# Performance work log

Measured on AMD Instinct MI355X. Metric: run time of the kernel, lower is better.

## Reference

```python
import jax, jax.numpy as jnp
import numpy as np

N = 100_000
E = 1_600_000
F_IN, D1, D2, D_EMB = 64, 32, 64, 64
NUM_GRAPHS = 16
BN_EPS = 1e-5


def _glorot(key, shape):
    fan_in, fan_out = shape[0], shape[1]
    lim = (6.0 / (fan_in + fan_out)) ** 0.5
    return jax.random.uniform(key, shape, jnp.float32, -lim, lim)


def setup_inputs() -> dict:
    key = jax.random.key(0)
    ks = jax.random.split(key, 12)
    x = jax.random.normal(ks[0], (N, F_IN), jnp.float32)
    edge_index = jax.random.randint(ks[1], (2, E), 0, N, jnp.int64)
    batch = jnp.sort(jax.random.randint(ks[2], (N,), 0, NUM_GRAPHS, jnp.int64))
    return {
        "x": x,
        "edge_index": edge_index,
        "batch": batch,
        "num_graphs": NUM_GRAPHS,
        "num_nodes": N,
        "W1a": _glorot(ks[3], (F_IN, D1)), "b1a": jnp.zeros((D1,), jnp.float32),
        "W1b": _glorot(ks[4], (D1, D2)), "b1b": jnp.zeros((D2,), jnp.float32),
        "g1": jnp.ones((D2,), jnp.float32), "be1": jnp.zeros((D2,), jnp.float32),
        "W2a": _glorot(ks[5], (D2, D2)), "b2a": jnp.zeros((D2,), jnp.float32),
        "W2b": _glorot(ks[6], (D2, D_EMB)), "b2b": jnp.zeros((D_EMB,), jnp.float32),
        "g2": jnp.ones((D_EMB,), jnp.float32), "be2": jnp.zeros((D_EMB,), jnp.float32),
    }


def _batchnorm_train(h, gamma, beta):
    mean = jnp.mean(h, axis=0)
    var = jnp.mean(jnp.square(h - mean), axis=0)  # biased var, as torch BN uses for normalization
    return (h - mean) * jax.lax.rsqrt(var + BN_EPS) * gamma + beta


def _gin_aggregate(x, src, dst, valid, n_nodes):
    # sum_{j in N(i)} x_j over valid edges only (masked scatter-add)
    msg = x[src] * valid[:, None]  # [E, D]
    return jax.ops.segment_sum(msg, dst, num_segments=n_nodes)


def reference(x, edge_index, batch, num_graphs, num_nodes,
              W1a, b1a, W1b, b1b, g1, be1,
              W2a, b2a, W2b, b2b, g2, be2):
    n_edges = edge_index.shape[1]
    per = n_edges // num_graphs
    # edge_mask: per-edge threshold g * num_nodes / num_graphs applied to both rows
    thresh = jnp.repeat(jnp.arange(num_graphs), per).astype(jnp.float32) * (num_nodes / num_graphs)
    valid = jnp.all(edge_index.astype(jnp.float32) - thresh[None, :] >= 0.0, axis=0)
    valid = valid.astype(x.dtype)
    src, dst = edge_index[0], edge_index[1]

    # GINConv 1 (eps=0): nn1(x + aggr)
    h = x + _gin_aggregate(x, src, dst, valid, num_nodes)
    h = jax.nn.relu(h @ W1a + b1a) @ W1b + b1b
    h = jax.nn.relu(h)
    h = _batchnorm_train(h, g1, be1)

    # GINConv 2
    h = h + _gin_aggregate(h, src, dst, valid, num_nodes)
    h = jax.nn.relu(h @ W2a + b2a) @ W2b + b2b
    h = jax.nn.relu(h)
    h = _batchnorm_train(h, g2, be2)

    # global_mean_pool
    sums = jax.ops.segment_sum(h, batch, num_segments=num_graphs)
    counts = jax.ops.segment_sum(jnp.ones((h.shape[0],), h.dtype), batch, num_segments=num_graphs)
    return sums / jnp.maximum(counts, 1.0)[:, None]
```

## Files before the change

### kernel.cpp

```cpp
#include <hip/hip_runtime.h>
#include <hip/hip_fp16.h>

#define NG 16
#define D 64
#define SLOT 32
#define NPB 128
#define INH 72

union HF4 { float4 f4; __half2 h2[4]; };
union HF2 { float2 f2; __half2 h2[2]; };

typedef _Float16 half4_t __attribute__((ext_vector_type(4)));
typedef float float4_t __attribute__((ext_vector_type(4)));

__device__ __forceinline__ float2 f2fma(float2 a, float2 b, float2 c) {
  return make_float2(fmaf(a.x, b.x, c.x), fmaf(a.y, b.y, c.y));
}
__device__ __forceinline__ float2 f2add(float2 a, float2 b) {
  return make_float2(a.x + b.x, a.y + b.y);
}

__device__ __forceinline__ void load16(const float4* __restrict__ feat4, int N,
                                       int q8, int4 a, int4 b, int4 c, int4 d,
                                       HF4* u) {
  int ix[16] = {a.x, a.y, a.z, a.w, b.x, b.y, b.z, b.w,
                c.x, c.y, c.z, c.w, d.x, d.y, d.z, d.w};
#pragma unroll
  for (int i = 0; i < 16; i++)
    u[i].f4 = feat4[(size_t)min(ix[i], N) * 8 + q8];
}
__device__ __forceinline__ void acc16(const HF4* u, float2* acc) {
#pragma unroll
  for (int i = 0; i < 16; i++) {
#pragma unroll
    for (int c = 0; c < 4; c++)
      acc[c] = f2add(acc[c], __half22float2(u[i].h2[c]));
  }
}

__global__ void prep_kernel(const float* __restrict__ x,
                            float2* __restrict__ xh, int n4,
                            float4* __restrict__ xz, float4* __restrict__ hz,
                            const int* __restrict__ ei,
                            int* __restrict__ fill, int* __restrict__ col,
                            int E, int per, int tmul) {
  int t = blockIdx.x * 256 + threadIdx.x;
  if (blockIdx.x == 0 && threadIdx.x < 16) {
    float4 z = make_float4(0.f, 0.f, 0.f, 0.f);
    if (threadIdx.x < 8) xz[threadIdx.x] = z;
    else hz[threadIdx.x - 8] = z;
  }
  if (t < n4) {
    float4 v = ((const float4*)x)[t];
    HF2 u;
    u.h2[0] = __floats2half2_rn(v.x, v.y);
    u.h2[1] = __floats2half2_rn(v.z, v.w);
    xh[t] = u.f2;
  }
  if (t < E) {
    int src = ei[t];
    int dst = ei[E + t];
    int thr = (t / per) * tmul;
    if (src >= thr && dst >= thr) {
      int k = atomicAdd(&fill[dst], 1);
      if (k < SLOT) col[dst * SLOT + k] = src;
    }
  }
}

template <int MID, bool FOLD_BN, int EPI>
__global__ __launch_bounds__(512, 2) void fused_layer_kernel(
    const float4* __restrict__ feat4,
    const int* __restrict__ col, const int* __restrict__ deg,
    const float* __restrict__ bn_sum, const float* __restrict__ bn_sq,
    const float* __restrict__ bn_gamma, const float* __restrict__ bn_beta,
    float invN,
    const float* __restrict__ Wa, const float* __restrict__ ba,
    const float* __restrict__ Wb, const float* __restrict__ bb,
    float2* __restrict__ out2,
    const int* __restrict__ batch,
    float* __restrict__ st_sum,
    float* __restrict__ st_sq,
    float* __restrict__ cnt,
    int N) {
  constexpr int CT = MID / 16;

  __shared__ __align__(16) __half s_h[NPB * INH];
  __shared__ __align__(16) __half s_wa[MID * 64];
  __shared__ __align__(16) __half s_wb[64 * MID];
  __shared__ __align__(16) float s_ba[MID];
  __shared__ __align__(16) float s_bb[D];
  __shared__ float s_bna[FOLD_BN ? D : 1];
  __shared__ float s_bnb[FOLD_BN ? D : 1];
  __shared__ int s_cnt[2];

  int tid = threadIdx.x;
  int base = blockIdx.x * NPB;

  {
    constexpr int WA_SLOTS = MID * 16;
    constexpr int WB_SLOTS = MID * 16;
    for (int g = tid; g < WA_SLOTS + WB_SLOTS; g += 512) {
      half4_t v;
      if (g < WA_SLOTS) {
        int l = g & 63, kt = (g >> 6) & 3, ct = g >> 8;
        int k0 = kt * 16 + ((l >> 4) << 2);
        int c = ct * 16 + (l & 15);
#pragma unroll
        for (int i = 0; i < 4; i++) v[i] = (_Float16)Wa[(k0 + i) * MID + c];
        *(half4_t*)&s_wa[g * 4] = v;
      } else {
        int g2 = g - WA_SLOTS;
        int l = g2 & 63;
        int kt = (g2 >> 6) & (CT - 1);
        int ot = g2 >> (6 + (CT == 4 ? 2 : 1));
        int k0 = kt * 16 + ((l >> 4) << 2);
        int o = ot * 16 + (l & 15);
#pragma unroll
        for (int i = 0; i < 4; i++) v[i] = (_Float16)Wb[(k0 + i) * D + o];
        *(half4_t*)&s_wb[g2 * 4] = v;
      }
    }
  }
  if (tid < MID) s_ba[tid] = ba[tid];
  if (tid < D) s_bb[tid] = bb[tid];
  if (FOLD_BN && tid < D) {
    float mean = bn_sum[tid] * invN;
    float var = bn_sq[tid] * invN - mean * mean;
    float av = bn_gamma[tid] * rsqrtf(var + 1e-5f);
    s_bna[tid] = av;
    s_bnb[tid] = bn_beta[tid] - mean * av;
  }
  if (EPI == 2 && tid < 2) s_cnt[tid] = 0;
  __syncthreads();

  {
    int q8 = tid & 7;
#pragma unroll
    for (int s0 = 0; s0 < 2; s0++) {
      int slot = (tid >> 3) + 64 * s0;
      int node = base + slot;
      float2 acc[4];
      if (node < N) {
        int d = min(deg[node], SLOT);
        const int4* cp = (const int4*)(col + (size_t)node * SLOT);
        {
          HF4 s; s.f4 = feat4[(size_t)node * 8 + q8];
#pragma unroll
          for (int i = 0; i < 4; i++) acc[i] = __half22float2(s.h2[i]);
        }
        HF4 u[16];
        load16(feat4, N, q8, cp[0], cp[1], cp[2], cp[3], u);
        acc16(u, acc);
        if (__any(d > 16)) {
          load16(feat4, N, q8, cp[4], cp[5], cp[6], cp[7], u);
          acc16(u, acc);
        }
        if (FOLD_BN) {
          float dp = (float)(d + 1);
          int c0 = q8 * 8;
#pragma unroll
          for (int c = 0; c < 4; c++) {
            float2 a2 = *(const float2*)&s_bna[c0 + 2 * c];
            float2 b2 = *(const float2*)&s_bnb[c0 + 2 * c];
            acc[c] = f2fma(a2, acc[c], make_float2(dp * b2.x, dp * b2.y));
          }
        }
      } else {
#pragma unroll
        for (int i = 0; i < 4; i++) acc[i] = make_float2(0.f, 0.f);
      }
      HF4 o;
#pragma unroll
      for (int c = 0; c < 4; c++)
        o.h2[c] = __floats2half2_rn(acc[c].x, acc[c].y);
      *(float4*)&s_h[slot * INH + q8 * 8] = o.f4;
    }
  }
  __syncthreads();

  int w = tid >> 6;
  int l = tid & 63;
  int lg = l >> 4;
  int ln = l & 15;
  int nodeB = base + w * 16 + ln;

  half4_t hb[4];
#pragma unroll
  for (int kt = 0; kt < 4; kt++)
    hb[kt] = *(const half4_t*)&s_h[(w * 16 + ln) * INH + kt * 16 + lg * 4];

  float4_t c1[CT];
#pragma unroll
  for (int ct = 0; ct < CT; ct++) {
    c1[ct] = *(const float4_t*)&s_ba[ct * 16 + lg * 4];
#pragma unroll
    for (int kt = 0; kt < 4; kt++) {
      half4_t a = *(const half4_t*)&s_wa[((ct * 4 + kt) * 64 + l) * 4];
      c1[ct] = __builtin_amdgcn_mfma_f32_16x16x16f16(a, hb[kt], c1[ct], 0, 0, 0);
    }
  }
  half4_t mb[CT];
#pragma unroll
  for (int ct = 0; ct < CT; ct++) {
#pragma unroll
    for (int r = 0; r < 4; r++) mb[ct][r] = (_Float16)fmaxf(c1[ct][r], 0.f);
  }
  float4_t o4[4];
#pragma unroll
  for (int ot = 0; ot < 4; ot++) {
    o4[ot] = *(const float4_t*)&s_bb[ot * 16 + lg * 4];
#pragma unroll
    for (int kt = 0; kt < CT; kt++) {
      half4_t a = *(const half4_t*)&s_wb[((ot * CT + kt) * 64 + l) * 4];
      o4[ot] = __builtin_amdgcn_mfma_f32_16x16x16f16(a, mb[kt], o4[ot], 0, 0, 0);
    }
#pragma unroll
    for (int r = 0; r < 4; r++) o4[ot][r] = fmaxf(o4[ot][r], 0.f);
  }

  float* red = (float*)s_h;

  if (EPI == 1) {
    bool val = nodeB < N;
    if (val) {
#pragma unroll
      for (int ot = 0; ot < 4; ot++) {
        HF2 u;
        u.h2[0] = __floats2half2_rn(o4[ot][0], o4[ot][1]);
        u.h2[1] = __floats2half2_rn(o4[ot][2], o4[ot][3]);
        out2[(size_t)nodeB * 16 + ot * 4 + lg] = u.f2;
      }
    }
    float vm = val ? 1.f : 0.f;
#pragma unroll
    for (int ot = 0; ot < 4; ot++) {
      float4_t s, q;
#pragma unroll
      for (int r = 0; r < 4; r++) {
        float x = vm * o4[ot][r];
        s[r] = x; q[r] = x * o4[ot][r];
      }
#pragma unroll
      for (int m = 1; m < 16; m <<= 1) {
#pragma unroll
        for (int r = 0; r < 4; r++) {
          s[r] += __shfl_xor(s[r], m);
          q[r] += __shfl_xor(q[r], m);
        }
      }
      if (ln == 0) {
        *(float4_t*)&red[w * 576 + ot * 16 + lg * 4] = s;
        *(float4_t*)&red[w * 576 + 64 + ot * 16 + lg * 4] = q;
      }
    }
    __syncthreads();
    if (tid < D) {
      float s = 0.f, q = 0.f;
#pragma unroll
      for (int ww = 0; ww < 8; ww++) {
        s += red[ww * 576 + tid];
        q += red[ww * 576 + 64 + tid];
      }
      atomicAdd(&st_sum[tid], s);
      atomicAdd(&st_sq[tid], q);
    }
  }

  if (EPI == 2) {
    bool val = nodeB < N;
    int bl = val ? batch[nodeB] : -1;
    int g_lo = batch[base];
    int g_hi = batch[min(base + NPB - 1, N - 1)];
    float vm = val ? 1.f : 0.f;
    float wlo = (bl == g_lo) ? 1.f : 0.f;
    unsigned long long mlo = __ballot(lg == 0 && bl == g_lo);
    unsigned long long mhi = __ballot(lg == 0 && val && bl != g_lo);
    if (l == 0) {
      atomicAdd(&s_cnt[0], (int)__popcll(mlo));
      atomicAdd(&s_cnt[1], (int)__popcll(mhi));
    }
#pragma unroll
    for (int ot = 0; ot < 4; ot++) {
      float4_t sl, st, sq;
#pragma unroll
      for (int r = 0; r < 4; r++) {
        float x = vm * o4[ot][r];
        sl[r] = wlo * x;
        st[r] = x;
        sq[r] = x * o4[ot][r];
      }
#pragma unroll
      for (int m = 1; m < 16; m <<= 1) {
#pragma unroll
        for (int r = 0; r < 4; r++) {
          sl[r] += __shfl_xor(sl[r], m);
          st[r] += __shfl_xor(st[r], m);
          sq[r] += __shfl_xor(sq[r], m);
        }
      }
      if (ln == 0) {
        *(float4_t*)&red[w * 576 + ot * 16 + lg * 4] = sl;
        float4_t sh;
#pragma unroll
        for (int r = 0; r < 4; r++) sh[r] = st[r] - sl[r];
        *(float4_t*)&red[w * 576 + 64 + ot * 16 + lg * 4] = sh;
        *(float4_t*)&red[w * 576 + 128 + ot * 16 + lg * 4] = sq;
      }
    }
    __syncthreads();
    if (tid < D) {
      float sl = 0.f, sh = 0.f, sq = 0.f;
#pragma unroll
      for (int ww = 0; ww < 8; ww++) {
        sl += red[ww * 576 + tid];
        sh += red[ww * 576 + 64 + tid];
        sq += red[ww * 576 + 128 + tid];
      }
      atomicAdd(&st_sum[g_lo * D + tid], sl);
      if (g_hi != g_lo) atomicAdd(&st_sum[g_hi * D + tid], sh);
      atomicAdd(&st_sq[tid], sq);
    }
    if (tid == 0) {
      atomicAdd(&cnt[g_lo], (float)s_cnt[0]);
      if (g_hi != g_lo) atomicAdd(&cnt[g_hi], (float)s_cnt[1]);
    }
  }
}

__global__ void final_kernel(const float* __restrict__ pool,
                             const float* __restrict__ cnt,
                             const float* __restrict__ sq,
                             const float* __restrict__ gamma,
                             const float* __restrict__ beta,
                             float invN, float* __restrict__ out) {
  int c = threadIdx.x;
  float s = 0.f;
#pragma unroll
  for (int g = 0; g < NG; g++) s += pool[g * D + c];
  float mean = s * invN;
  float var = sq[c] * invN - mean * mean;
  float a = gamma[c] * rsqrtf(var + 1e-5f);
  float b = beta[c] - mean * a;
#pragma unroll
  for (int g = 0; g < NG; g++) {
    float n = cnt[g];
    out[g * D + c] = (a * pool[g * D + c] + n * b) / fmaxf(n, 1.f);
  }
}

extern "C" void kernel_launch(void* const* d_in, const int* in_sizes, int n_in,
                              void* d_out, int out_size, void* d_ws, size_t ws_size,
                              hipStream_t stream) {
  const float* x   = (const float*)d_in[0];
  const int* ei    = (const int*)d_in[1];
  const int* batch = (const int*)d_in[2];
  const float* W1a = (const float*)d_in[5];
  const float* b1a = (const float*)d_in[6];
  const float* W1b = (const float*)d_in[7];
  const float* b1b = (const float*)d_in[8];
  const float* g1  = (const float*)d_in[9];
  const float* be1 = (const float*)d_in[10];
  const float* W2a = (const float*)d_in[11];
  const float* b2a = (const float*)d_in[12];
  const float* W2b = (const float*)d_in[13];
  const float* b2b = (const float*)d_in[14];
  const float* g2  = (const float*)d_in[15];
  const float* be2 = (const float*)d_in[16];

  int N = in_sizes[0] / D;
  int E = in_sizes[1] / 2;
  int per = E / NG;
  int tmul = N / NG;
  float invN = 1.f / (float)N;

  float* ws = (float*)d_ws;
  size_t ndh = (size_t)(N + 1) * D / 2;
  float* h1h = ws;
  float* xh  = ws + ndh;
  int*   col = (int*)(ws + 2 * ndh);
  float* stats = ws + 2 * ndh + (size_t)N * SLOT;
  float* sum1 = stats;
  float* sq1  = stats + 64;
  float* pool = stats + 128;
  float* cnt  = stats + 128 + NG * D;
  float* sq2  = stats + 144 + NG * D;
  int*   fill = (int*)(stats + 208 + NG * D);

  hipMemsetAsync(stats, 0, (208 + NG * D + N) * sizeof(float), stream);
  hipMemsetAsync(col, 0x7F, (size_t)N * SLOT * sizeof(int), stream);

  int n4 = N * D / 4;
  int pgrid = (max(n4, E) + 255) / 256;
  prep_kernel<<<pgrid, 256, 0, stream>>>(
      x, (float2*)xh, n4,
      (float4*)(xh + (size_t)N * D / 2),
      (float4*)(h1h + (size_t)N * D / 2),
      ei, fill, col, E, per, tmul);

  int fblocks = (N + NPB - 1) / NPB;

  fused_layer_kernel<32, false, 1><<<fblocks, 512, 0, stream>>>(
      (const float4*)xh, col, fill, nullptr, nullptr, nullptr, nullptr, invN,
      W1a, b1a, W1b, b1b, (float2*)h1h, nullptr, sum1, sq1, nullptr, N);

  fused_layer_kernel<64, true, 2><<<fblocks, 512, 0, stream>>>(
      (const float4*)h1h, col, fill, sum1, sq1, g1, be1, invN,
      W2a, b2a, W2b, b2b, nullptr, batch, pool, sq2, cnt, N);

  final_kernel<<<1, 64, 0, stream>>>(pool, cnt, sq2, g2, be2, invN, (float*)d_out);
}
```

Baseline: 221.1 us.

## Drop block-level barriers by per-wave atomics into banked stat accumulators

Each wave now builds only its own 16 rows of the aggregated tile in shared memory, so the block-wide barrier before the MFMA stage becomes a wave-local LDS wait. The shared-memory cross-wave reduction and its second barrier in both epilogues are removed. Each wave instead issues global atomics directly into 16 banked copies of the BN sum/sq accumulators, chosen by wave index and block parity, and per-wave graph boundaries are used for pooling. Readers sum the banks afterwards. This trades block synchronisation for roughly eight times more global atomics, spread over banks to reduce contention.

```diff
diff --git a/kernel.cpp b/kernel.cpp
--- a/kernel.cpp
+++ b/kernel.cpp
@@ -6,6 +6,7 @@
 #define SLOT 32
 #define NPB 128
 #define INH 72
+#define NBANK 16
 
 union HF4 { float4 f4; __half2 h2[4]; };
 union HF2 { float2 f2; __half2 h2[2]; };
@@ -18,6 +19,11 @@
 }
 __device__ __forceinline__ float2 f2add(float2 a, float2 b) {
   return make_float2(a.x + b.x, a.y + b.y);
+}
+__device__ __forceinline__ float pick4(float4_t v, int k) {
+  float a = (k & 1) ? v[1] : v[0];
+  float b = (k & 1) ? v[3] : v[2];
+  return (k & 2) ? b : a;
 }
 
 __device__ __forceinline__ void load16(const float4* __restrict__ feat4, int N,
@@ -92,9 +98,10 @@
   __shared__ __align__(16) float s_bb[D];
   __shared__ float s_bna[FOLD_BN ? D : 1];
   __shared__ float s_bnb[FOLD_BN ? D : 1];
-  __shared__ int s_cnt[2];
 
   int tid = threadIdx.x;
+  int w = tid >> 6;
+  int l = tid & 63;
   int base = blockIdx.x * NPB;
 
   {
@@ -103,19 +110,19 @@
     for (int g = tid; g < WA_SLOTS + WB_SLOTS; g += 512) {
       half4_t v;
       if (g < WA_SLOTS) {
-        int l = g & 63, kt = (g >> 6) & 3, ct = g >> 8;
-        int k0 = kt * 16 + ((l >> 4) << 2);
-        int c = ct * 16 + (l & 15);
+        int ll = g & 63, kt = (g >> 6) & 3, ct = g >> 8;
+        int k0 = kt * 16 + ((ll >> 4) << 2);
+        int c = ct * 16 + (ll & 15);
 #pragma unroll
         for (int i = 0; i < 4; i++) v[i] = (_Float16)Wa[(k0 + i) * MID + c];
         *(half4_t*)&s_wa[g * 4] = v;
       } else {
         int g2 = g - WA_SLOTS;
-        int l = g2 & 63;
+        int ll = g2 & 63;
         int kt = (g2 >> 6) & (CT - 1);
         int ot = g2 >> (6 + (CT == 4 ? 2 : 1));
-        int k0 = kt * 16 + ((l >> 4) << 2);
-        int o = ot * 16 + (l & 15);
+        int k0 = kt * 16 + ((ll >> 4) << 2);
+        int o = ot * 16 + (ll & 15);
 #pragma unroll
         for (int i = 0; i < 4; i++) v[i] = (_Float16)Wb[(k0 + i) * D + o];
         *(half4_t*)&s_wb[g2 * 4] = v;
@@ -125,21 +132,26 @@
   if (tid < MID) s_ba[tid] = ba[tid];
   if (tid < D) s_bb[tid] = bb[tid];
   if (FOLD_BN && tid < D) {
-    float mean = bn_sum[tid] * invN;
-    float var = bn_sq[tid] * invN - mean * mean;
+    float s = 0.f, q = 0.f;
+#pragma unroll
+    for (int b = 0; b < NBANK; b++) {
+      s += bn_sum[b * D + tid];
+      q += bn_sq[b * D + tid];
+    }
+    float mean = s * invN;
+    float var = q * invN - mean * mean;
     float av = bn_gamma[tid] * rsqrtf(var + 1e-5f);
     s_bna[tid] = av;
     s_bnb[tid] = bn_beta[tid] - mean * av;
   }
-  if (EPI == 2 && tid < 2) s_cnt[tid] = 0;
   __syncthreads();
 
   {
-    int q8 = tid & 7;
+    int q8 = l & 7;
 #pragma unroll
     for (int s0 = 0; s0 < 2; s0++) {
-      int slot = (tid >> 3) + 64 * s0;
-      int node = base + slot;
+      int r = w * 16 + s0 * 8 + (l >> 3);
+      int node = base + r;
       float2 acc[4];
       if (node < N) {
         int d = min(deg[node], SLOT);
@@ -174,13 +186,12 @@
 #pragma unroll
       for (int c = 0; c < 4; c++)
         o.h2[c] = __floats2half2_rn(acc[c].x, acc[c].y);
-      *(float4*)&s_h[slot * INH + q8 * 8] = o.f4;
-    }
-  }
-  __syncthreads();
-
-  int w = tid >> 6;
-  int l = tid & 63;
+      *(float4*)&s_h[r * INH + q8 * 8] = o.f4;
+    }
+  }
+  asm volatile("s_waitcnt lgkmcnt(0)" ::: "memory");
+  __builtin_amdgcn_sched_barrier(0);
+
   int lg = l >> 4;
   int ln = l & 15;
   int nodeB = base + w * 16 + ln;
@@ -219,10 +230,11 @@
     for (int r = 0; r < 4; r++) o4[ot][r] = fmaxf(o4[ot][r], 0.f);
   }
 
-  float* red = (float*)s_h;
+  bool val = nodeB < N;
+  float vm = val ? 1.f : 0.f;
+  int bank = ((blockIdx.x & 1) << 3) | w;
 
   if (EPI == 1) {
-    bool val = nodeB < N;
     if (val) {
 #pragma unroll
       for (int ot = 0; ot < 4; ot++) {
@@ -232,7 +244,6 @@
         out2[(size_t)nodeB * 16 + ot * 4 + lg] = u.f2;
       }
     }
-    float vm = val ? 1.f : 0.f;
 #pragma unroll
     for (int ot = 0; ot < 4; ot++) {
       float4_t s, q;
@@ -249,36 +260,23 @@
           q[r] += __shfl_xor(q[r], m);
         }
       }
-      if (ln == 0) {
-        *(float4_t*)&red[w * 576 + ot * 16 + lg * 4] = s;
-        *(float4_t*)&red[w * 576 + 64 + ot * 16 + lg * 4] = q;
-      }
-    }
-    __syncthreads();
-    if (tid < D) {
-      float s = 0.f, q = 0.f;
-#pragma unroll
-      for (int ww = 0; ww < 8; ww++) {
-        s += red[ww * 576 + tid];
-        q += red[ww * 576 + 64 + tid];
-      }
-      atomicAdd(&st_sum[tid], s);
-      atomicAdd(&st_sq[tid], q);
+      int k = ln & 3;
+      float v = (ln < 4) ? pick4(s, k) : pick4(q, k);
+      float* p = ((ln < 4) ? st_sum : st_sq) + bank * D + ot * 16 + lg * 4 + k;
+      if (ln < 8) atomicAdd(p, v);
     }
   }
 
   if (EPI == 2) {
-    bool val = nodeB < N;
+    int g_lo = batch[min(base + w * 16, N - 1)];
+    int g_hi = batch[min(base + w * 16 + 15, N - 1)];
     int bl = val ? batch[nodeB] : -1;
-    int g_lo = batch[base];
-    int g_hi = batch[min(base + NPB - 1, N - 1)];
-    float vm = val ? 1.f : 0.f;
     float wlo = (bl == g_lo) ? 1.f : 0.f;
-    unsigned long long mlo = __ballot(lg == 0 && bl == g_lo);
+    unsigned long long mlo = __ballot(lg == 0 && val && bl == g_lo);
     unsigned long long mhi = __ballot(lg == 0 && val && bl != g_lo);
     if (l == 0) {
-      atomicAdd(&s_cnt[0], (int)__popcll(mlo));
-      atomicAdd(&s_cnt[1], (int)__popcll(mhi));
+      atomicAdd(&cnt[g_lo], (float)__popcll(mlo));
+      if (g_hi != g_lo) atomicAdd(&cnt[g_hi], (float)__popcll(mhi));
     }
 #pragma unroll
     for (int ot = 0; ot < 4; ot++) {
@@ -299,31 +297,17 @@
           sq[r] += __shfl_xor(sq[r], m);
         }
       }
-      if (ln == 0) {
-        *(float4_t*)&red[w * 576 + ot * 16 + lg * 4] = sl;
-        float4_t sh;
-#pragma unroll
-        for (int r = 0; r < 4; r++) sh[r] = st[r] - sl[r];
-        *(float4_t*)&red[w * 576 + 64 + ot * 16 + lg * 4] = sh;
-        *(float4_t*)&red[w * 576 + 128 + ot * 16 + lg * 4] = sq;
-      }
-    }
-    __syncthreads();
-    if (tid < D) {
-      float sl = 0.f, sh = 0.f, sq = 0.f;
-#pragma unroll
-      for (int ww = 0; ww < 8; ww++) {
-        sl += red[ww * 576 + tid];
-        sh += red[ww * 576 + 64 + tid];
-        sq += red[ww * 576 + 128 + tid];
-      }
-      atomicAdd(&st_sum[g_lo * D + tid], sl);
-      if (g_hi != g_lo) atomicAdd(&st_sum[g_hi * D + tid], sh);
-      atomicAdd(&st_sq[tid], sq);
-    }
-    if (tid == 0) {
-      atomicAdd(&cnt[g_lo], (float)s_cnt[0]);
-      if (g_hi != g_lo) atomicAdd(&cnt[g_hi], (float)s_cnt[1]);
+      int k = ln & 3, grp = ln >> 2;
+      float vlo = pick4(sl, k);
+      float vhi = pick4(st, k) - vlo;
+      float vsq = pick4(sq, k);
+      float v = (grp == 0) ? vlo : (grp == 1) ? vhi : vsq;
+      int c = ot * 16 + lg * 4 + k;
+      float* p = (grp == 0) ? &st_sum[g_lo * D + c]
+               : (grp == 1) ? &st_sum[g_hi * D + c]
+                            : &st_sq[bank * D + c];
+      bool act = (ln < 12) && !(grp == 1 && g_hi == g_lo);
+      if (act) atomicAdd(p, v);
     }
   }
 }
@@ -338,8 +322,11 @@
   float s = 0.f;
 #pragma unroll
   for (int g = 0; g < NG; g++) s += pool[g * D + c];
+  float q = 0.f;
+#pragma unroll
+  for (int b = 0; b < NBANK; b++) q += sq[b * D + c];
   float mean = s * invN;
-  float var = sq[c] * invN - mean * mean;
+  float var = q * invN - mean * mean;
   float a = gamma[c] * rsqrtf(var + 1e-5f);
   float b = beta[c] - mean * a;
 #pragma unroll
@@ -381,13 +368,14 @@
   int*   col = (int*)(ws + 2 * ndh);
   float* stats = ws + 2 * ndh + (size_t)N * SLOT;
   float* sum1 = stats;
-  float* sq1  = stats + 64;
-  float* pool = stats + 128;
-  float* cnt  = stats + 128 + NG * D;
-  float* sq2  = stats + 144 + NG * D;
-  int*   fill = (int*)(stats + 208 + NG * D);
-
-  hipMemsetAsync(stats, 0, (208 + NG * D + N) * sizeof(float), stream);
+  float* sq1  = stats + NBANK * D;
+  float* pool = stats + 2 * NBANK * D;
+  float* cnt  = pool + NG * D;
+  float* sq2  = cnt + NG;
+  int*   fill = (int*)(sq2 + NBANK * D);
+  size_t nstat = 3 * NBANK * D + NG * D + NG;
+
+  hipMemsetAsync(stats, 0, (nstat + N) * sizeof(float), stream);
   hipMemsetAsync(col, 0x7F, (size_t)N * SLOT * sizeof(int), stream);
 
   int n4 = N * D / 4;
```

Result: slower. 268.1 us (+21.3%).

## Merge col memset into zero memset with +1 index encoding and vectorize prep

Applied to the files above, without the earlier changes.

Neighbor indices are now stored as src+1 so a zero-filled adjacency slot maps, via an unsigned wraparound and clamp, to the zero row at index N. This lets the col table be cleared by the same single zeroing memset as the stats and fill counters, so the separate 0x7F memset goes away. The prep kernel also now handles four elements per thread, using int4 loads for edge indices and a grid-stride loop for the fp16 conversion, which shrinks the grid. Edge counts not divisible by four would drop the tail edges, and the loader adds an extra subtract per gather.

```diff
diff --git a/kernel.cpp b/kernel.cpp
--- a/kernel.cpp
+++ b/kernel.cpp
@@ -26,8 +26,10 @@
   int ix[16] = {a.x, a.y, a.z, a.w, b.x, b.y, b.z, b.w,
                 c.x, c.y, c.z, c.w, d.x, d.y, d.z, d.w};
 #pragma unroll
-  for (int i = 0; i < 16; i++)
-    u[i].f4 = feat4[(size_t)min(ix[i], N) * 8 + q8];
+  for (int i = 0; i < 16; i++) {
+    unsigned r = (unsigned)(ix[i] - 1);
+    u[i].f4 = feat4[(size_t)min(r, (unsigned)N) * 8 + q8];
+  }
 }
 __device__ __forceinline__ void acc16(const HF4* u, float2* acc) {
 #pragma unroll
@@ -45,25 +47,37 @@
                             int* __restrict__ fill, int* __restrict__ col,
                             int E, int per, int tmul) {
   int t = blockIdx.x * 256 + threadIdx.x;
+  int T = gridDim.x * 256;
   if (blockIdx.x == 0 && threadIdx.x < 16) {
     float4 z = make_float4(0.f, 0.f, 0.f, 0.f);
     if (threadIdx.x < 8) xz[threadIdx.x] = z;
     else hz[threadIdx.x - 8] = z;
   }
-  if (t < n4) {
-    float4 v = ((const float4*)x)[t];
-    HF2 u;
-    u.h2[0] = __floats2half2_rn(v.x, v.y);
-    u.h2[1] = __floats2half2_rn(v.z, v.w);
-    xh[t] = u.f2;
-  }
-  if (t < E) {
-    int src = ei[t];
-    int dst = ei[E + t];
-    int thr = (t / per) * tmul;
-    if (src >= thr && dst >= thr) {
-      int k = atomicAdd(&fill[dst], 1);
-      if (k < SLOT) col[dst * SLOT + k] = src;
+  const float4* x4 = (const float4*)x;
+#pragma unroll
+  for (int i = 0; i < 4; i++) {
+    int idx = i * T + t;
+    if (idx < n4) {
+      float4 v = x4[idx];
+      HF2 u;
+      u.h2[0] = __floats2half2_rn(v.x, v.y);
+      u.h2[1] = __floats2half2_rn(v.z, v.w);
+      xh[idx] = u.f2;
+    }
+  }
+  int e0 = 4 * t;
+  if (e0 + 3 < E) {
+    int4 s4 = *(const int4*)(ei + e0);
+    int4 d4 = *(const int4*)(ei + E + e0);
+    int thr = (e0 / per) * tmul;
+    int ss[4] = {s4.x, s4.y, s4.z, s4.w};
+    int dd[4] = {d4.x, d4.y, d4.z, d4.w};
+#pragma unroll
+    for (int i = 0; i < 4; i++) {
+      if (ss[i] >= thr && dd[i] >= thr) {
+        int k = atomicAdd(&fill[dd[i]], 1);
+        if (k < SLOT) col[dd[i] * SLOT + k] = ss[i] + 1;
+      }
     }
   }
 }
@@ -378,20 +392,21 @@
   size_t ndh = (size_t)(N + 1) * D / 2;
   float* h1h = ws;
   float* xh  = ws + ndh;
-  int*   col = (int*)(ws + 2 * ndh);
-  float* stats = ws + 2 * ndh + (size_t)N * SLOT;
+  float* stats = ws + 2 * ndh;
   float* sum1 = stats;
   float* sq1  = stats + 64;
   float* pool = stats + 128;
   float* cnt  = stats + 128 + NG * D;
   float* sq2  = stats + 144 + NG * D;
   int*   fill = (int*)(stats + 208 + NG * D);
-
-  hipMemsetAsync(stats, 0, (208 + NG * D + N) * sizeof(float), stream);
-  hipMemsetAsync(col, 0x7F, (size_t)N * SLOT * sizeof(int), stream);
+  int*   col  = fill + N;
+  size_t zwords = (size_t)(208 + NG * D) + N + (size_t)N * SLOT;
+
+  hipMemsetAsync(stats, 0, zwords * sizeof(float), stream);
 
   int n4 = N * D / 4;
-  int pgrid = (max(n4, E) + 255) / 256;
+  int tot4 = (max(n4, E) + 3) / 4;
+  int pgrid = (tot4 + 255) / 256;
   prep_kernel<<<pgrid, 256, 0, stream>>>(
       x, (float2*)xh, n4,
       (float4*)(xh + (size_t)N * D / 2),
```

After: 233.5 us. 5.6% more time.
